# Kernel optimization log

Measured on AMD Instinct MI355X. Metric: run time of the kernel, lower is better.

Reference implementation:

```python
import jax, jax.numpy as jnp
import numpy as np

B, T, H = 2048, 512, 64  # batch, seq_len, hidden_size


def setup_inputs() -> dict:
    key = jax.random.key(0)
    ks = jax.random.split(key, 12)
    s = 1.0 / np.sqrt(H)  # PyTorch default uniform init bound
    u = lambda k, shape: jax.random.uniform(k, shape, jnp.float32, -s, s)
    return {
        "x": jax.random.normal(ks[0], (B, T), dtype=jnp.float32),
        # layer 0: input_size=1
        "w_ih0": u(ks[1], (4 * H, 1)),
        "w_hh0": u(ks[2], (4 * H, H)),
        "b_ih0": u(ks[3], (4 * H,)),
        "b_hh0": u(ks[4], (4 * H,)),
        # layer 1: input_size=H
        "w_ih1": u(ks[5], (4 * H, H)),
        "w_hh1": u(ks[6], (4 * H, H)),
        "b_ih1": u(ks[7], (4 * H,)),
        "b_hh1": u(ks[8], (4 * H,)),
        # final projection 64 -> 1
        "fc_w": u(ks[9], (1, H)),
        "fc_b": u(ks[10], (1,)),
    }


def _lstm_layer(x, w_ih, w_hh, b_ih, b_hh):
    """x: [B, T, D] -> hidden states [B, T, H]. PyTorch gate order i,f,g,o."""
    bsz = x.shape[0]
    # input contribution for all timesteps at once: [B, T, 4H]
    gx = jnp.einsum('btd,gd->btg', x, w_ih) + b_ih + b_hh
    gx = jnp.swapaxes(gx, 0, 1)  # time-major [T, B, 4H]

    def step(carry, g_t):
        h, c = carry
        g = g_t + h @ w_hh.T  # [B, 4H]
        i, f, gg, o = jnp.split(g, 4, axis=-1)
        i = jax.nn.sigmoid(i)
        f = jax.nn.sigmoid(f)
        gg = jnp.tanh(gg)
        o = jax.nn.sigmoid(o)
        c = f * c + i * gg
        h = o * jnp.tanh(c)
        return (h, c), h

    h0 = jnp.zeros((bsz, H), dtype=x.dtype)
    _, hs = jax.lax.scan(step, (h0, h0), gx)
    return jnp.swapaxes(hs, 0, 1)  # [B, T, H]


def reference(x, w_ih0, w_hh0, b_ih0, b_hh0, w_ih1, w_hh1, b_ih1, b_hh1, fc_w, fc_b):
    x3 = x[..., None]  # unsqueeze(2): [B, T, 1]
    h1 = _lstm_layer(x3, w_ih0, w_hh0, b_ih0, b_hh0)
    h2 = _lstm_layer(h1, w_ih1, w_hh1, b_ih1, b_hh1)
    # fc applied to last timestep of layer-2 output
    return h2[:, -1, :] @ fc_w.T + fc_b  # [B, 1]
```

## Files before the change

### kernel.cpp

```cpp
#include <hip/hip_runtime.h>

#define TLEN 512
#define HDIM 64
#define NB   8
#define NTH  512
#define GRID 256

typedef __attribute__((ext_vector_type(8))) short bf16x8;
typedef __attribute__((ext_vector_type(4))) float f32x4;

__device__ __forceinline__ float sigm(float x){ return __fdividef(1.f, 1.f+__expf(-x)); }
__device__ __forceinline__ float tanh_(float x){ return 1.f - __fdividef(2.f, __expf(2.f*x)+1.f); }

__device__ __forceinline__ short bf16rn(float f){
    unsigned u = __float_as_uint(f);
    u = (u + 0x7FFFu + ((u >> 16) & 1u)) >> 16;
    return (short)u;
}
__device__ __forceinline__ float bf2f(short s){
    return __uint_as_float(((unsigned)(unsigned short)s) << 16);
}

__device__ __forceinline__ void loadA(const float* __restrict__ W, int rowbase, int lane,
                                      bf16x8& hi0, bf16x8& lo0, bf16x8& hi1, bf16x8& lo1)
{
    const int row = rowbase + (lane & 15);
    const int q   = lane >> 4;
    const float* p = W + row * HDIM + q * 8;
    #pragma unroll
    for (int e = 0; e < 8; ++e) {
        const float f0 = p[e];
        const float f1 = p[32 + e];
        const short a0 = bf16rn(f0); hi0[e] = a0; lo0[e] = bf16rn(f0 - bf2f(a0));
        const short a1 = bf16rn(f1); hi1[e] = a1; lo1[e] = bf16rn(f1 - bf2f(a1));
    }
}

__global__ __launch_bounds__(NTH, 2)
void lstm2_mfma(const float* __restrict__ x,
                const float* __restrict__ w_ih0,
                const float* __restrict__ w_hh0,
                const float* __restrict__ b_ih0,
                const float* __restrict__ b_hh0,
                const float* __restrict__ w_ih1,
                const float* __restrict__ w_hh1,
                const float* __restrict__ b_ih1,
                const float* __restrict__ b_hh1,
                const float* __restrict__ fc_w,
                const float* __restrict__ fc_b,
                float* __restrict__ out)
{
    __shared__ float xs[NB][TLEN];
    __shared__ float gates[3 * 256 * 9];
    __shared__ __align__(16) short h1hi[16][72];
    __shared__ __align__(16) short h1lo[16][72];
    __shared__ __align__(16) short h2hi[16][72];
    __shared__ __align__(16) short h2lo[16][72];
    __shared__ float h2last[NB * HDIM];

    const int tid  = threadIdx.x;
    const int wid  = tid >> 6;
    const int lane = tid & 63;
    const int q    = lane >> 4;
    const int r15  = lane & 15;
    const int b0   = blockIdx.x * NB;

    {
        const float4* xg = (const float4*)(x + (size_t)b0 * TLEN);
        for (int idx = tid; idx < NB * TLEN / 4; idx += NTH) {
            const int row = idx >> 7;
            const int col = idx & 127;
            ((float4*)&xs[row][0])[col] = xg[row * 128 + col];
        }
    }
    for (int idx = tid; idx < 16 * 72; idx += NTH) {
        ((short*)h1hi)[idx] = 0; ((short*)h1lo)[idx] = 0;
        ((short*)h2hi)[idx] = 0; ((short*)h2lo)[idx] = 0;
    }

    bf16x8 Ahi0[6], Alo0[6], Ahi1[6], Alo1[6];
    const int rb_lo = wid * 16;
    const int rb_hi = wid * 16 + 128;
    loadA(w_hh0, rb_lo, lane, Ahi0[0], Alo0[0], Ahi1[0], Alo1[0]);
    loadA(w_hh0, rb_hi, lane, Ahi0[1], Alo0[1], Ahi1[1], Alo1[1]);
    loadA(w_ih1, rb_lo, lane, Ahi0[2], Alo0[2], Ahi1[2], Alo1[2]);
    loadA(w_ih1, rb_hi, lane, Ahi0[3], Alo0[3], Ahi1[3], Alo1[3]);
    loadA(w_hh1, rb_lo, lane, Ahi0[4], Alo0[4], Ahi1[4], Alo1[4]);
    loadA(w_hh1, rb_hi, lane, Ahi0[5], Alo0[5], Ahi1[5], Alo1[5]);

    f32x4 biasf[6];
    #pragma unroll
    for (int j = 0; j < 6; ++j) {
        const int rb = (wid + 8 * (j & 1)) * 16 + q * 4;
        #pragma unroll
        for (int r = 0; r < 4; ++r) {
            float bv = 0.f;
            if (j < 2)      bv = b_ih0[rb + r] + b_hh0[rb + r];
            else if (j < 4) bv = b_ih1[rb + r] + b_hh1[rb + r];
            biasf[j][r] = bv;
        }
    }

    const int ub = tid >> 6;
    const int uk = tid & 63;
    const float wx0 = w_ih0[uk];
    const float wx1 = w_ih0[64  + uk];
    const float wx2 = w_ih0[128 + uk];
    const float wx3 = w_ih0[192 + uk];
    float c1 = 0.f, c2 = 0.f;

    __syncthreads();

    for (int i = 0; i <= TLEN; ++i) {
        const bf16x8 B1h0 = *(const bf16x8*)&h1hi[r15][q * 8];
        const bf16x8 B1h1 = *(const bf16x8*)&h1hi[r15][32 + q * 8];
        const bf16x8 B1l0 = *(const bf16x8*)&h1lo[r15][q * 8];
        const bf16x8 B1l1 = *(const bf16x8*)&h1lo[r15][32 + q * 8];
        const bf16x8 B2h0 = *(const bf16x8*)&h2hi[r15][q * 8];
        const bf16x8 B2h1 = *(const bf16x8*)&h2hi[r15][32 + q * 8];
        const bf16x8 B2l0 = *(const bf16x8*)&h2lo[r15][q * 8];
        const bf16x8 B2l1 = *(const bf16x8*)&h2lo[r15][32 + q * 8];

        #pragma unroll
        for (int j = 0; j < 6; ++j) {
            const bf16x8 bh0 = (j < 4) ? B1h0 : B2h0;
            const bf16x8 bh1 = (j < 4) ? B1h1 : B2h1;
            const bf16x8 bl0 = (j < 4) ? B1l0 : B2l0;
            const bf16x8 bl1 = (j < 4) ? B1l1 : B2l1;
            f32x4 acc = biasf[j];
            acc = __builtin_amdgcn_mfma_f32_16x16x32_bf16(Ahi0[j], bh0, acc, 0, 0, 0);
            acc = __builtin_amdgcn_mfma_f32_16x16x32_bf16(Ahi1[j], bh1, acc, 0, 0, 0);
            acc = __builtin_amdgcn_mfma_f32_16x16x32_bf16(Alo0[j], bh0, acc, 0, 0, 0);
            acc = __builtin_amdgcn_mfma_f32_16x16x32_bf16(Alo1[j], bh1, acc, 0, 0, 0);
            acc = __builtin_amdgcn_mfma_f32_16x16x32_bf16(Ahi0[j], bl0, acc, 0, 0, 0);
            acc = __builtin_amdgcn_mfma_f32_16x16x32_bf16(Ahi1[j], bl1, acc, 0, 0, 0);
            acc = __builtin_amdgcn_mfma_f32_16x16x32_bf16(Alo0[j], bl0, acc, 0, 0, 0);
            acc = __builtin_amdgcn_mfma_f32_16x16x32_bf16(Alo1[j], bl1, acc, 0, 0, 0);
            if (r15 < NB) {
                const int growbase = (j >> 1) * 256 + (wid + 8 * (j & 1)) * 16 + q * 4;
                #pragma unroll
                for (int r = 0; r < 4; ++r)
                    gates[(growbase + r) * 9 + r15] = acc[r];
            }
        }
        __syncthreads();

        if (i < TLEN) {
            const float xv = xs[ub][i];
            const float p0 = gates[(      uk) * 9 + ub] + wx0 * xv;
            const float p1 = gates[( 64 + uk) * 9 + ub] + wx1 * xv;
            const float p2 = gates[(128 + uk) * 9 + ub] + wx2 * xv;
            const float p3 = gates[(192 + uk) * 9 + ub] + wx3 * xv;
            const float gi = sigm(p0), gf = sigm(p1), gg = tanh_(p2), go = sigm(p3);
            c1 = fmaf(gf, c1, gi * gg);
            const float h1v = go * tanh_(c1);
            const short hh = bf16rn(h1v);
            h1hi[ub][uk] = hh;
            h1lo[ub][uk] = bf16rn(h1v - bf2f(hh));
        }
        if (i >= 1) {
            const float p0 = gates[(256 +       uk) * 9 + ub] + gates[(512 +       uk) * 9 + ub];
            const float p1 = gates[(256 +  64 + uk) * 9 + ub] + gates[(512 +  64 + uk) * 9 + ub];
            const float p2 = gates[(256 + 128 + uk) * 9 + ub] + gates[(512 + 128 + uk) * 9 + ub];
            const float p3 = gates[(256 + 192 + uk) * 9 + ub] + gates[(512 + 192 + uk) * 9 + ub];
            const float gi = sigm(p0), gf = sigm(p1), gg = tanh_(p2), go = sigm(p3);
            c2 = fmaf(gf, c2, gi * gg);
            const float h2v = go * tanh_(c2);
            const short hh = bf16rn(h2v);
            h2hi[ub][uk] = hh;
            h2lo[ub][uk] = bf16rn(h2v - bf2f(hh));
            if (i == TLEN) h2last[ub * HDIM + uk] = h2v;
        }
        __syncthreads();
    }

    {
        float p = fc_w[uk] * h2last[ub * HDIM + uk];
        #pragma unroll
        for (int off = 32; off; off >>= 1) p += __shfl_down(p, off, 64);
        if (uk == 0) out[b0 + ub] = p + fc_b[0];
    }
}

extern "C" void kernel_launch(void* const* d_in, const int* in_sizes, int n_in,
                              void* d_out, int out_size, void* d_ws, size_t ws_size,
                              hipStream_t stream) {
    const float* xp     = (const float*)d_in[0];
    const float* w_ih0  = (const float*)d_in[1];
    const float* w_hh0  = (const float*)d_in[2];
    const float* b_ih0  = (const float*)d_in[3];
    const float* b_hh0  = (const float*)d_in[4];
    const float* w_ih1  = (const float*)d_in[5];
    const float* w_hh1  = (const float*)d_in[6];
    const float* b_ih1  = (const float*)d_in[7];
    const float* b_hh1  = (const float*)d_in[8];
    const float* fc_w   = (const float*)d_in[9];
    const float* fc_b   = (const float*)d_in[10];
    float* outp = (float*)d_out;

    lstm2_mfma<<<dim3(GRID), dim3(NTH), 0, stream>>>(
        xp, w_ih0, w_hh0, b_ih0, b_hh0,
        w_ih1, w_hh1, b_ih1, b_hh1, fc_w, fc_b, outp);
}
```

Measured before the change: 944.2 us.

## Warp-specialize LSTM layers, fuse gate activations into MFMA lanes, double-buffer hidden state

```diff
diff --git a/kernel.cpp b/kernel.cpp
--- a/kernel.cpp
+++ b/kernel.cpp
@@ -2,11 +2,13 @@
 
 #define TLEN 512
 #define HDIM 64
-#define NB   8
+#define NB   16
 #define NTH  512
-#define GRID 256
+#define GRID 128
+#define XPAD 516
 
 typedef __attribute__((ext_vector_type(8))) short bf16x8;
+typedef __attribute__((ext_vector_type(4))) short short4v;
 typedef __attribute__((ext_vector_type(4))) float f32x4;
 
 __device__ __forceinline__ float sigm(float x){ return __fdividef(1.f, 1.f+__expf(-x)); }
@@ -36,27 +38,26 @@
     }
 }
 
+#define MFMA __builtin_amdgcn_mfma_f32_16x16x32_bf16
+
 __global__ __launch_bounds__(NTH, 2)
-void lstm2_mfma(const float* __restrict__ x,
-                const float* __restrict__ w_ih0,
-                const float* __restrict__ w_hh0,
-                const float* __restrict__ b_ih0,
-                const float* __restrict__ b_hh0,
-                const float* __restrict__ w_ih1,
-                const float* __restrict__ w_hh1,
-                const float* __restrict__ b_ih1,
-                const float* __restrict__ b_hh1,
-                const float* __restrict__ fc_w,
-                const float* __restrict__ fc_b,
-                float* __restrict__ out)
+void lstm2_ws(const float* __restrict__ x,
+              const float* __restrict__ w_ih0,
+              const float* __restrict__ w_hh0,
+              const float* __restrict__ b_ih0,
+              const float* __restrict__ b_hh0,
+              const float* __restrict__ w_ih1,
+              const float* __restrict__ w_hh1,
+              const float* __restrict__ b_ih1,
+              const float* __restrict__ b_hh1,
+              const float* __restrict__ fc_w,
+              const float* __restrict__ fc_b,
+              float* __restrict__ out)
 {
-    __shared__ float xs[NB][TLEN];
-    __shared__ float gates[3 * 256 * 9];
-    __shared__ __align__(16) short h1hi[16][72];
-    __shared__ __align__(16) short h1lo[16][72];
-    __shared__ __align__(16) short h2hi[16][72];
-    __shared__ __align__(16) short h2lo[16][72];
-    __shared__ float h2last[NB * HDIM];
+    __shared__ float xs[NB * XPAD];
+    __shared__ short h1f[2][2][2][4][16][8];
+    __shared__ short h2f[2][2][2][4][16][8];
+    __shared__ float h2last[NB][HDIM];
 
     const int tid  = threadIdx.x;
     const int wid  = tid >> 6;
@@ -64,121 +65,152 @@
     const int q    = lane >> 4;
     const int r15  = lane & 15;
     const int b0   = blockIdx.x * NB;
+    const bool isL0 = (wid < 4);
 
     {
         const float4* xg = (const float4*)(x + (size_t)b0 * TLEN);
         for (int idx = tid; idx < NB * TLEN / 4; idx += NTH) {
             const int row = idx >> 7;
             const int col = idx & 127;
-            ((float4*)&xs[row][0])[col] = xg[row * 128 + col];
-        }
-    }
-    for (int idx = tid; idx < 16 * 72; idx += NTH) {
-        ((short*)h1hi)[idx] = 0; ((short*)h1lo)[idx] = 0;
-        ((short*)h2hi)[idx] = 0; ((short*)h2lo)[idx] = 0;
-    }
-
-    bf16x8 Ahi0[6], Alo0[6], Ahi1[6], Alo1[6];
-    const int rb_lo = wid * 16;
-    const int rb_hi = wid * 16 + 128;
-    loadA(w_hh0, rb_lo, lane, Ahi0[0], Alo0[0], Ahi1[0], Alo1[0]);
-    loadA(w_hh0, rb_hi, lane, Ahi0[1], Alo0[1], Ahi1[1], Alo1[1]);
-    loadA(w_ih1, rb_lo, lane, Ahi0[2], Alo0[2], Ahi1[2], Alo1[2]);
-    loadA(w_ih1, rb_hi, lane, Ahi0[3], Alo0[3], Ahi1[3], Alo1[3]);
-    loadA(w_hh1, rb_lo, lane, Ahi0[4], Alo0[4], Ahi1[4], Alo1[4]);
-    loadA(w_hh1, rb_hi, lane, Ahi0[5], Alo0[5], Ahi1[5], Alo1[5]);
-
-    f32x4 biasf[6];
-    #pragma unroll
-    for (int j = 0; j < 6; ++j) {
-        const int rb = (wid + 8 * (j & 1)) * 16 + q * 4;
-        #pragma unroll
-        for (int r = 0; r < 4; ++r) {
-            float bv = 0.f;
-            if (j < 2)      bv = b_ih0[rb + r] + b_hh0[rb + r];
-            else if (j < 4) bv = b_ih1[rb + r] + b_hh1[rb + r];
-            biasf[j][r] = bv;
-        }
-    }
-
-    const int ub = tid >> 6;
-    const int uk = tid & 63;
-    const float wx0 = w_ih0[uk];
-    const float wx1 = w_ih0[64  + uk];
-    const float wx2 = w_ih0[128 + uk];
-    const float wx3 = w_ih0[192 + uk];
-    float c1 = 0.f, c2 = 0.f;
+            *(float4*)&xs[row * XPAD + col * 4] = xg[row * 128 + col];
+        }
+    }
+    for (int idx = tid; idx < 8192; idx += NTH) {
+        ((short*)h1f)[idx] = 0;
+        ((short*)h2f)[idx] = 0;
+    }
+
+    const int w4 = isL0 ? wid : (wid - 4);
+    const int U0 = w4 * 16;
+    bf16x8 M0h0[4], M0l0[4], M0h1[4], M0l1[4];
+    bf16x8 M1h0[4], M1l0[4], M1h1[4], M1l1[4];
+    f32x4 biasv[4], wih[4];
+    if (isL0) {
+        #pragma unroll
+        for (int g = 0; g < 4; ++g)
+            loadA(w_hh0, g * 64 + U0, lane, M0h0[g], M0l0[g], M0h1[g], M0l1[g]);
+        #pragma unroll
+        for (int g = 0; g < 4; ++g) {
+            #pragma unroll
+            for (int r = 0; r < 4; ++r) {
+                const int row = g * 64 + U0 + q * 4 + r;
+                biasv[g][r] = b_ih0[row] + b_hh0[row];
+                wih[g][r]   = w_ih0[row];
+            }
+        }
+    } else {
+        #pragma unroll
+        for (int g = 0; g < 4; ++g) {
+            loadA(w_ih1, g * 64 + U0, lane, M0h0[g], M0l0[g], M0h1[g], M0l1[g]);
+            loadA(w_hh1, g * 64 + U0, lane, M1h0[g], M1l0[g], M1h1[g], M1l1[g]);
+        }
+        #pragma unroll
+        for (int g = 0; g < 4; ++g) {
+            #pragma unroll
+            for (int r = 0; r < 4; ++r) {
+                const int row = g * 64 + U0 + q * 4 + r;
+                biasv[g][r] = b_ih1[row] + b_hh1[row];
+                wih[g][r]   = 0.f;
+            }
+        }
+    }
+    const int kh = w4 >> 1;
+    const int qp = (2 * w4 + (q >> 1)) & 3;
+    const int eo = (q & 1) * 4;
+    f32x4 cc = {0.f, 0.f, 0.f, 0.f};
+    int p = 0;
 
     __syncthreads();
 
     for (int i = 0; i <= TLEN; ++i) {
-        const bf16x8 B1h0 = *(const bf16x8*)&h1hi[r15][q * 8];
-        const bf16x8 B1h1 = *(const bf16x8*)&h1hi[r15][32 + q * 8];
-        const bf16x8 B1l0 = *(const bf16x8*)&h1lo[r15][q * 8];
-        const bf16x8 B1l1 = *(const bf16x8*)&h1lo[r15][32 + q * 8];
-        const bf16x8 B2h0 = *(const bf16x8*)&h2hi[r15][q * 8];
-        const bf16x8 B2h1 = *(const bf16x8*)&h2hi[r15][32 + q * 8];
-        const bf16x8 B2l0 = *(const bf16x8*)&h2lo[r15][q * 8];
-        const bf16x8 B2l1 = *(const bf16x8*)&h2lo[r15][32 + q * 8];
-
-        #pragma unroll
-        for (int j = 0; j < 6; ++j) {
-            const bf16x8 bh0 = (j < 4) ? B1h0 : B2h0;
-            const bf16x8 bh1 = (j < 4) ? B1h1 : B2h1;
-            const bf16x8 bl0 = (j < 4) ? B1l0 : B2l0;
-            const bf16x8 bl1 = (j < 4) ? B1l1 : B2l1;
-            f32x4 acc = biasf[j];
-            acc = __builtin_amdgcn_mfma_f32_16x16x32_bf16(Ahi0[j], bh0, acc, 0, 0, 0);
-            acc = __builtin_amdgcn_mfma_f32_16x16x32_bf16(Ahi1[j], bh1, acc, 0, 0, 0);
-            acc = __builtin_amdgcn_mfma_f32_16x16x32_bf16(Alo0[j], bh0, acc, 0, 0, 0);
-            acc = __builtin_amdgcn_mfma_f32_16x16x32_bf16(Alo1[j], bh1, acc, 0, 0, 0);
-            acc = __builtin_amdgcn_mfma_f32_16x16x32_bf16(Ahi0[j], bl0, acc, 0, 0, 0);
-            acc = __builtin_amdgcn_mfma_f32_16x16x32_bf16(Ahi1[j], bl1, acc, 0, 0, 0);
-            acc = __builtin_amdgcn_mfma_f32_16x16x32_bf16(Alo0[j], bl0, acc, 0, 0, 0);
-            acc = __builtin_amdgcn_mfma_f32_16x16x32_bf16(Alo1[j], bl1, acc, 0, 0, 0);
-            if (r15 < NB) {
-                const int growbase = (j >> 1) * 256 + (wid + 8 * (j & 1)) * 16 + q * 4;
+        const bool active = isL0 ? (i < TLEN) : (i >= 1);
+        if (active) {
+            f32x4 acc[4];
+            if (isL0) {
+                const bf16x8 Bh0 = *(const bf16x8*)&h1f[p][0][0][q][r15][0];
+                const bf16x8 Bh1 = *(const bf16x8*)&h1f[p][0][1][q][r15][0];
+                const bf16x8 Bl0 = *(const bf16x8*)&h1f[p][1][0][q][r15][0];
+                const bf16x8 Bl1 = *(const bf16x8*)&h1f[p][1][1][q][r15][0];
+                const float xv = xs[r15 * XPAD + i];
                 #pragma unroll
-                for (int r = 0; r < 4; ++r)
-                    gates[(growbase + r) * 9 + r15] = acc[r];
+                for (int g = 0; g < 4; ++g) {
+                    f32x4 a = biasv[g];
+                    #pragma unroll
+                    for (int r = 0; r < 4; ++r) a[r] = fmaf(wih[g][r], xv, a[r]);
+                    a = MFMA(M0h0[g], Bh0, a, 0, 0, 0);
+                    a = MFMA(M0h1[g], Bh1, a, 0, 0, 0);
+                    a = MFMA(M0l0[g], Bh0, a, 0, 0, 0);
+                    a = MFMA(M0l1[g], Bh1, a, 0, 0, 0);
+                    a = MFMA(M0h0[g], Bl0, a, 0, 0, 0);
+                    a = MFMA(M0h1[g], Bl1, a, 0, 0, 0);
+                    acc[g] = a;
+                }
+            } else {
+                const bf16x8 B1h0 = *(const bf16x8*)&h1f[p][0][0][q][r15][0];
+                const bf16x8 B1h1 = *(const bf16x8*)&h1f[p][0][1][q][r15][0];
+                const bf16x8 B1l0 = *(const bf16x8*)&h1f[p][1][0][q][r15][0];
+                const bf16x8 B1l1 = *(const bf16x8*)&h1f[p][1][1][q][r15][0];
+                const bf16x8 B2h0 = *(const bf16x8*)&h2f[p][0][0][q][r15][0];
+                const bf16x8 B2h1 = *(const bf16x8*)&h2f[p][0][1][q][r15][0];
+                const bf16x8 B2l0 = *(const bf16x8*)&h2f[p][1][0][q][r15][0];
+                const bf16x8 B2l1 = *(const bf16x8*)&h2f[p][1][1][q][r15][0];
+                #pragma unroll
+                for (int g = 0; g < 4; ++g) {
+                    f32x4 a = biasv[g];
+                    a = MFMA(M0h0[g], B1h0, a, 0, 0, 0);
+                    a = MFMA(M0h1[g], B1h1, a, 0, 0, 0);
+                    a = MFMA(M0l0[g], B1h0, a, 0, 0, 0);
+                    a = MFMA(M0l1[g], B1h1, a, 0, 0, 0);
+                    a = MFMA(M0h0[g], B1l0, a, 0, 0, 0);
+                    a = MFMA(M0h1[g], B1l1, a, 0, 0, 0);
+                    f32x4 h = {0.f, 0.f, 0.f, 0.f};
+                    h = MFMA(M1h0[g], B2h0, h, 0, 0, 0);
+                    h = MFMA(M1h1[g], B2h1, h, 0, 0, 0);
+                    h = MFMA(M1l0[g], B2h0, h, 0, 0, 0);
+                    h = MFMA(M1l1[g], B2h1, h, 0, 0, 0);
+                    h = MFMA(M1h0[g], B2l0, h, 0, 0, 0);
+                    h = MFMA(M1h1[g], B2l1, h, 0, 0, 0);
+                    #pragma unroll
+                    for (int r = 0; r < 4; ++r) acc[g][r] = a[r] + h[r];
+                }
+            }
+            float hv[4];
+            #pragma unroll
+            for (int r = 0; r < 4; ++r) {
+                const float gi = sigm (acc[0][r]);
+                const float gf = sigm (acc[1][r]);
+                const float gg = tanh_(acc[2][r]);
+                const float go = sigm (acc[3][r]);
+                cc[r] = fmaf(gf, cc[r], gi * gg);
+                hv[r] = go * tanh_(cc[r]);
+            }
+            const short hh0 = bf16rn(hv[0]), hl0 = bf16rn(hv[0] - bf2f(hh0));
+            const short hh1 = bf16rn(hv[1]), hl1 = bf16rn(hv[1] - bf2f(hh1));
+            const short hh2 = bf16rn(hv[2]), hl2 = bf16rn(hv[2] - bf2f(hh2));
+            const short hh3 = bf16rn(hv[3]), hl3 = bf16rn(hv[3] - bf2f(hh3));
+            if (isL0) {
+                *(short4v*)&h1f[p ^ 1][0][kh][qp][r15][eo] = (short4v){hh0, hh1, hh2, hh3};
+                *(short4v*)&h1f[p ^ 1][1][kh][qp][r15][eo] = (short4v){hl0, hl1, hl2, hl3};
+            } else {
+                *(short4v*)&h2f[p ^ 1][0][kh][qp][r15][eo] = (short4v){hh0, hh1, hh2, hh3};
+                *(short4v*)&h2f[p ^ 1][1][kh][qp][r15][eo] = (short4v){hl0, hl1, hl2, hl3};
+                if (i == TLEN)
+                    *(f32x4*)&h2last[r15][U0 + q * 4] = (f32x4){hv[0], hv[1], hv[2], hv[3]};
             }
         }
         __syncthreads();
-
-        if (i < TLEN) {
-            const float xv = xs[ub][i];
-            const float p0 = gates[(      uk) * 9 + ub] + wx0 * xv;
-            const float p1 = gates[( 64 + uk) * 9 + ub] + wx1 * xv;
-            const float p2 = gates[(128 + uk) * 9 + ub] + wx2 * xv;
-            const float p3 = gates[(192 + uk) * 9 + ub] + wx3 * xv;
-            const float gi = sigm(p0), gf = sigm(p1), gg = tanh_(p2), go = sigm(p3);
-            c1 = fmaf(gf, c1, gi * gg);
-            const float h1v = go * tanh_(c1);
-            const short hh = bf16rn(h1v);
-            h1hi[ub][uk] = hh;
-            h1lo[ub][uk] = bf16rn(h1v - bf2f(hh));
-        }
-        if (i >= 1) {
-            const float p0 = gates[(256 +       uk) * 9 + ub] + gates[(512 +       uk) * 9 + ub];
-            const float p1 = gates[(256 +  64 + uk) * 9 + ub] + gates[(512 +  64 + uk) * 9 + ub];
-            const float p2 = gates[(256 + 128 + uk) * 9 + ub] + gates[(512 + 128 + uk) * 9 + ub];
-            const float p3 = gates[(256 + 192 + uk) * 9 + ub] + gates[(512 + 192 + uk) * 9 + ub];
-            const float gi = sigm(p0), gf = sigm(p1), gg = tanh_(p2), go = sigm(p3);
-            c2 = fmaf(gf, c2, gi * gg);
-            const float h2v = go * tanh_(c2);
-            const short hh = bf16rn(h2v);
-            h2hi[ub][uk] = hh;
-            h2lo[ub][uk] = bf16rn(h2v - bf2f(hh));
-            if (i == TLEN) h2last[ub * HDIM + uk] = h2v;
-        }
-        __syncthreads();
+        p ^= 1;
     }
 
     {
-        float p = fc_w[uk] * h2last[ub * HDIM + uk];
-        #pragma unroll
-        for (int off = 32; off; off >>= 1) p += __shfl_down(p, off, 64);
-        if (uk == 0) out[b0 + ub] = p + fc_b[0];
+        const int fb = tid >> 5, fs = tid & 31;
+        float psum = fc_w[fs] * h2last[fb][fs] + fc_w[fs + 32] * h2last[fb][fs + 32];
+        psum += __shfl_xor(psum, 16);
+        psum += __shfl_xor(psum, 8);
+        psum += __shfl_xor(psum, 4);
+        psum += __shfl_xor(psum, 2);
+        psum += __shfl_xor(psum, 1);
+        if (fs == 0) out[b0 + fb] = psum + fc_b[0];
     }
 }
 
@@ -198,7 +230,7 @@
     const float* fc_b   = (const float*)d_in[10];
     float* outp = (float*)d_out;
 
-    lstm2_mfma<<<dim3(GRID), dim3(NTH), 0, stream>>>(
+    lstm2_ws<<<dim3(GRID), dim3(NTH), 0, stream>>>(
         xp, w_ih0, w_hh0, b_ih0, b_hh0,
         w_ih1, w_hh1, b_ih1, b_hh1, fc_w, fc_b, outp);
 }
```

Measured after the change: 1.058 ms. +12.0%, slower.
